# Kernel optimization log

Hardware: AMD Instinct MI355X
Metric: run time of the kernel (lower is better)

The kernel has to match this reference:

```python
import jax, jax.numpy as jnp
import numpy as np

D_IN = 1024
D_OUT = 1024
NUM_HEADS = 16
HEAD_DIM = D_OUT // NUM_HEADS


def setup_inputs() -> dict:
    key = jax.random.key(0)
    ks = jax.random.split(key, 6)
    scale = 0.02
    x = jax.random.normal(ks[0], (2, 2048, D_IN), dtype=jnp.float32)
    Wq = jax.random.normal(ks[1], (D_IN, D_OUT), dtype=jnp.float32) * scale
    Wk = jax.random.normal(ks[2], (D_IN, D_OUT), dtype=jnp.float32) * scale
    Wv = jax.random.normal(ks[3], (D_IN, D_OUT), dtype=jnp.float32) * scale
    Wo = jax.random.normal(ks[4], (D_OUT, D_OUT), dtype=jnp.float32) * scale
    bo = jax.random.normal(ks[5], (D_OUT,), dtype=jnp.float32) * scale
    return {"x": x, "Wq": Wq, "Wk": Wk, "Wv": Wv, "Wo": Wo, "bo": bo}


def reference(x, Wq, Wk, Wv, Wo, bo):
    b, T, _ = x.shape
    h, dh = NUM_HEADS, HEAD_DIM
    # QKV projections (no bias), split heads: [b,T,d_out] -> [b,h,T,dh]
    q = (x @ Wq).reshape(b, T, h, dh).transpose(0, 2, 1, 3)
    k = (x @ Wk).reshape(b, T, h, dh).transpose(0, 2, 1, 3)
    v = (x @ Wv).reshape(b, T, h, dh).transpose(0, 2, 1, 3)
    # scaled dot-product scores with causal mask
    scores = jnp.einsum("bhqd,bhkd->bhqk", q, k) / jnp.sqrt(jnp.float32(dh))
    causal = jnp.tril(jnp.ones((T, T), dtype=bool))  # True = allowed
    scores = jnp.where(causal, scores, -jnp.inf)
    attn = jax.nn.softmax(scores, axis=-1)
    # dropout p=0.0 -> identity
    ctx = jnp.einsum("bhqk,bhkd->bhqd", attn, v)
    ctx = ctx.transpose(0, 2, 1, 3).reshape(b, T, h * dh)
    return ctx @ Wo + bo
```

## Files before the change

### kernel.cpp

```cpp
#include <hip/hip_runtime.h>

typedef __attribute__((ext_vector_type(8))) __bf16 bf16x8;
typedef __attribute__((ext_vector_type(4))) __bf16 bf16x4;
typedef __attribute__((ext_vector_type(4))) float  f32x4;

static constexpr int TSEQ    = 2048;
static constexpr int DMODEL  = 1024;
static constexpr int HD      = 64;
static constexpr int VSTRIDE = 2080;
static constexpr int LSTR    = 72;

#define AS1 __attribute__((address_space(1)))
#define AS3 __attribute__((address_space(3)))

__global__ __launch_bounds__(256) void k_prep(const float* __restrict__ x,
    const float* __restrict__ w0, const float* __restrict__ w1,
    const float* __restrict__ w2, const float* __restrict__ w3,
    __bf16* __restrict__ xbf, __bf16* __restrict__ wt_all) {
  __shared__ float tile[32][33];
  const int blk = blockIdx.x;
  const int tid = threadIdx.x;
  if (blk < 4096) {
    size_t i = ((size_t)blk * 256 + tid) * 4;
    float4 v = *(const float4*)(x + i);
    bf16x4 o = { (__bf16)v.x, (__bf16)v.y, (__bf16)v.z, (__bf16)v.w };
    *(bf16x4*)(xbf + i) = o;
    return;
  }
  const int tz = blk - 4096;
  const int wi = tz >> 10;
  const int tl = tz & 1023;
  const int n0 = (tl & 31) * 32, k0 = (tl >> 5) * 32;
  const float* w = wi == 0 ? w0 : wi == 1 ? w1 : wi == 2 ? w2 : w3;
  __bf16* out = wt_all + (size_t)wi * DMODEL * DMODEL;
  const int tx = tid & 31, ty0 = (tid >> 5) * 4;
#pragma unroll
  for (int j = 0; j < 4; j++)
    tile[ty0 + j][tx] = w[(size_t)(k0 + ty0 + j) * DMODEL + n0 + tx];
  __syncthreads();
#pragma unroll
  for (int j = 0; j < 4; j++)
    out[(size_t)(n0 + ty0 + j) * DMODEL + k0 + tx] = (__bf16)tile[tx][ty0 + j];
}

template <int NB>
__device__ __forceinline__ void gemm_mainloop_p(const __bf16* __restrict__ A,
                                                const __bf16* __restrict__ Bt,
                                                int bm, int bn,
                                                __bf16* At, __bf16* Bl,
                                                f32x4 acc[4][NB / 32]) {
  constexpr int NT = NB / 32;
  const int tid  = threadIdx.x;
  const int lane = tid & 63;
  const int l15  = lane & 15, quad = lane >> 4;
  const int wv   = tid >> 6;
  const int wm   = (wv >> 1) * 64, wn = (wv & 1) * (NT * 16);
  const int srow = lane >> 2;
  const int scol = (((lane & 3) ^ ((lane >> 3) & 3)) << 3);
  const int rsw  = (l15 >> 1) & 3;

  auto stage = [&](int k0, int hb) {
#pragma unroll
    for (int ss = 0; ss < 2; ss++) {
      const int s   = wv * 2 + ss;
      const int row = s * 16 + srow;
      __builtin_amdgcn_global_load_lds(
          (const AS1 void*)(A + (size_t)(bm + row) * 1024 + k0 + scol),
          (AS3 void*)(At + hb * 4096 + s * 512), 16, 0, 0);
    }
#pragma unroll
    for (int ss = 0; ss < NB / 64; ss++) {
      const int s   = wv * (NB / 64) + ss;
      const int row = s * 16 + srow;
      __builtin_amdgcn_global_load_lds(
          (const AS1 void*)(Bt + (size_t)(bn + row) * 1024 + k0 + scol),
          (AS3 void*)(Bl + hb * (NB * 32) + s * 512), 16, 0, 0);
    }
  };

  stage(0, 0);
  for (int k0 = 0; k0 < 1024; k0 += 32) {
    const int cur = (k0 >> 5) & 1;
    __syncthreads();
    bf16x8 af[4], bfr[NT];
#pragma unroll
    for (int mt = 0; mt < 4; mt++)
      af[mt] = *(const bf16x8*)(At + cur * 4096 + (wm + mt * 16 + l15) * 32 +
                                ((quad ^ rsw) << 3));
#pragma unroll
    for (int nt = 0; nt < NT; nt++)
      bfr[nt] = *(const bf16x8*)(Bl + cur * (NB * 32) + (wn + nt * 16 + l15) * 32 +
                                 ((quad ^ rsw) << 3));
    if (k0 + 32 < 1024) stage(k0 + 32, cur ^ 1);
#pragma unroll
    for (int mt = 0; mt < 4; mt++)
#pragma unroll
      for (int nt = 0; nt < NT; nt++)
        acc[mt][nt] = __builtin_amdgcn_mfma_f32_16x16x32_bf16(
            af[mt], bfr[nt], acc[mt][nt], 0, 0, 0);
  }
}

__global__ __launch_bounds__(256) void k_gemm_qkv(const __bf16* __restrict__ xbf,
    const __bf16* __restrict__ wt_all, __bf16* __restrict__ qws,
    __bf16* __restrict__ kws, __bf16* __restrict__ vtws) {
  __shared__ __bf16 At[2 * 128 * 32];
  __shared__ __bf16 Bl[2 * 128 * 32];
  const int which = blockIdx.z;
  const __bf16* wt = wt_all + (size_t)which * DMODEL * DMODEL;
  const int bm = blockIdx.y * 128, bn = blockIdx.x * 128;
  f32x4 acc[4][4];
  const f32x4 z = {0.f, 0.f, 0.f, 0.f};
#pragma unroll
  for (int mt = 0; mt < 4; mt++)
#pragma unroll
    for (int nt = 0; nt < 4; nt++) acc[mt][nt] = z;
  gemm_mainloop_p<128>(xbf, wt, bm, bn, At, Bl, acc);
  const int lane = threadIdx.x & 63;
  const int l15 = lane & 15, quad = lane >> 4;
  const int wv = threadIdx.x >> 6;
  const int wm = (wv >> 1) * 64, wn = (wv & 1) * 64;
  if (which == 2) {
#pragma unroll
    for (int mt = 0; mt < 4; mt++)
#pragma unroll
      for (int nt = 0; nt < 4; nt++) {
        int t0 = bm + wm + mt * 16 + quad * 4;
        int n = bn + wn + nt * 16 + l15;
        int h = n >> 6, d = n & 63;
        int b = t0 >> 11;
        int bh = b * 16 + h;
        bf16x4 o = { (__bf16)acc[mt][nt][0], (__bf16)acc[mt][nt][1],
                     (__bf16)acc[mt][nt][2], (__bf16)acc[mt][nt][3] };
        *(bf16x4*)(vtws + ((size_t)bh * HD + d) * VSTRIDE + (t0 & 2047)) = o;
      }
  } else {
#pragma unroll
    for (int mt = 0; mt < 4; mt++)
#pragma unroll
      for (int nt = 0; nt < 4; nt++)
#pragma unroll
        for (int r = 0; r < 4; r++) {
          int m = bm + wm + mt * 16 + quad * 4 + r;
          int n = bn + wn + nt * 16 + l15;
          int b = m >> 11, t = m & 2047;
          int h = n >> 6,  d = n & 63;
          int bh = b * 16 + h;
          float av = acc[mt][nt][r];
          if (which == 0) qws[((size_t)bh * TSEQ + t) * HD + d] = (__bf16)(av * 0.18033688f);
          else            kws[((size_t)bh * TSEQ + t) * HD + d] = (__bf16)av;
        }
  }
}

__global__ __launch_bounds__(256) void k_attn(const __bf16* __restrict__ qws,
    const __bf16* __restrict__ kws, const __bf16* __restrict__ vtws,
    __bf16* __restrict__ ctx) {
  const int bh  = blockIdx.x & 31;
  const int qb0 = blockIdx.x >> 5, qb1 = 31 - qb0;
  const int tid = threadIdx.x;
  const int lane = tid & 63, wv = tid >> 6;
  const int l15 = lane & 15, quad = lane >> 4;
  const __bf16* qp = qws  + (size_t)bh * TSEQ * HD;
  const __bf16* kp = kws  + (size_t)bh * TSEQ * HD;
  const __bf16* vp = vtws + (size_t)bh * HD * VSTRIDE;
  const int b = bh >> 4, h = bh & 15;

  __shared__ __bf16 kbuf[2][64 * LSTR];
  __shared__ __bf16 vbuf[2][64 * LSTR];
  __shared__ __bf16 plds[4][16 * LSTR];

  const f32x4 z = {0.f, 0.f, 0.f, 0.f};
  const int sr = tid >> 3, sc = (tid & 7) * 8;

  const int qr0a = qb0 * 64 + wv * 16;
  const int qr0b = qb1 * 64 + wv * 16;
  bf16x8 aq0[2], aq1[2];
#pragma unroll
  for (int kb = 0; kb < 2; kb++) {
    aq0[kb] = *(const bf16x8*)(qp + (size_t)(qr0a + l15) * HD + kb * 32 + quad * 8);
    aq1[kb] = *(const bf16x8*)(qp + (size_t)(qr0b + l15) * HD + kb * 32 + quad * 8);
  }

  bf16x8 kreg[2], vreg[2];
  kreg[0] = *(const bf16x8*)(kp + (size_t)sr * HD + sc);
  kreg[1] = *(const bf16x8*)(kp + (size_t)(sr + 32) * HD + sc);
  vreg[0] = *(const bf16x8*)(vp + (size_t)sr * VSTRIDE + sc);
  vreg[1] = *(const bf16x8*)(vp + (size_t)(sr + 32) * VSTRIDE + sc);
  *(bf16x8*)(kbuf[0] + sr * LSTR + sc)        = kreg[0];
  *(bf16x8*)(kbuf[0] + (sr + 32) * LSTR + sc) = kreg[1];
  *(bf16x8*)(vbuf[0] + sr * LSTR + sc)        = vreg[0];
  *(bf16x8*)(vbuf[0] + (sr + 32) * LSTR + sc) = vreg[1];
  __syncthreads();

  float lpart[4] = {0.f, 0.f, 0.f, 0.f};
  f32x4 acc[4];
#pragma unroll
  for (int dt = 0; dt < 4; dt++) acc[dt] = z;

  for (int s = 0; s < 33; s++) {
    const int cur = s & 1;
    const bool h0 = (s <= qb0);
    const bool masked = (s == qb0) || (s == 32);

    if (s + 1 < 33) {
      const int ktn = (s + 1 <= qb0) ? (s + 1) * 64 : (s - qb0) * 64;
      kreg[0] = *(const bf16x8*)(kp + (size_t)(ktn + sr) * HD + sc);
      kreg[1] = *(const bf16x8*)(kp + (size_t)(ktn + sr + 32) * HD + sc);
      vreg[0] = *(const bf16x8*)(vp + (size_t)sr * VSTRIDE + ktn + sc);
      vreg[1] = *(const bf16x8*)(vp + (size_t)(sr + 32) * VSTRIDE + ktn + sc);
    }

    const __bf16* kb_ = kbuf[cur];
    const __bf16* vb_ = vbuf[cur];
    f32x4 sarr[4];
#pragma unroll
    for (int nt = 0; nt < 4; nt++) sarr[nt] = z;
#pragma unroll
    for (int nt = 0; nt < 4; nt++)
#pragma unroll
      for (int kb = 0; kb < 2; kb++) {
        bf16x8 bk = *(const bf16x8*)(kb_ + (nt * 16 + l15) * LSTR + kb * 32 + quad * 8);
        bf16x8 a  = h0 ? aq0[kb] : aq1[kb];
        sarr[nt] = __builtin_amdgcn_mfma_f32_16x16x32_bf16(a, bk, sarr[nt], 0, 0, 0);
      }
    if (masked) {
#pragma unroll
      for (int r = 0; r < 4; r++) {
        const int qloc = wv * 16 + quad * 4 + r;
#pragma unroll
        for (int nt = 0; nt < 4; nt++) {
          int kloc = nt * 16 + l15;
          float p = (kloc <= qloc) ? __builtin_amdgcn_exp2f(sarr[nt][r]) : 0.f;
          lpart[r] += p;
          plds[wv][(quad * 4 + r) * LSTR + nt * 16 + l15] = (__bf16)p;
        }
      }
    } else {
#pragma unroll
      for (int r = 0; r < 4; r++)
#pragma unroll
        for (int nt = 0; nt < 4; nt++) {
          float p = __builtin_amdgcn_exp2f(sarr[nt][r]);
          lpart[r] += p;
          plds[wv][(quad * 4 + r) * LSTR + nt * 16 + l15] = (__bf16)p;
        }
    }
#pragma unroll
    for (int kb = 0; kb < 2; kb++) {
      bf16x8 ap = *(const bf16x8*)(&plds[wv][l15 * LSTR + kb * 32 + quad * 8]);
#pragma unroll
      for (int dt = 0; dt < 4; dt++) {
        bf16x8 bvv = *(const bf16x8*)(vb_ + (dt * 16 + l15) * LSTR + kb * 32 + quad * 8);
        acc[dt] = __builtin_amdgcn_mfma_f32_16x16x32_bf16(ap, bvv, acc[dt], 0, 0, 0);
      }
    }

    if (s + 1 < 33) {
      const int nxt = cur ^ 1;
      *(bf16x8*)(kbuf[nxt] + sr * LSTR + sc)        = kreg[0];
      *(bf16x8*)(kbuf[nxt] + (sr + 32) * LSTR + sc) = kreg[1];
      *(bf16x8*)(vbuf[nxt] + sr * LSTR + sc)        = vreg[0];
      *(bf16x8*)(vbuf[nxt] + (sr + 32) * LSTR + sc) = vreg[1];
    }
    __syncthreads();

    if (masked) {
      const int qr0 = h0 ? qr0a : qr0b;
#pragma unroll
      for (int r = 0; r < 4; r++) {
        float l = lpart[r];
        l += __shfl_xor(l, 1, 64);
        l += __shfl_xor(l, 2, 64);
        l += __shfl_xor(l, 4, 64);
        l += __shfl_xor(l, 8, 64);
        float linv = 1.f / l;
        const int qrow = qr0 + quad * 4 + r;
#pragma unroll
        for (int dt = 0; dt < 4; dt++)
          ctx[((size_t)(b * TSEQ + qrow)) * DMODEL + h * 64 + dt * 16 + l15] =
              (__bf16)(acc[dt][r] * linv);
        lpart[r] = 0.f;
      }
#pragma unroll
      for (int dt = 0; dt < 4; dt++) acc[dt] = z;
    }
  }
}

__global__ __launch_bounds__(256) void k_gemm_out(const __bf16* __restrict__ ctx,
    const __bf16* __restrict__ wot, const float* __restrict__ bo,
    float* __restrict__ out) {
  __shared__ __bf16 At[2 * 128 * 32];
  __shared__ __bf16 Bl[2 * 64 * 32];
  const int bm = blockIdx.y * 128, bn = blockIdx.x * 64;
  f32x4 acc[4][2];
  const f32x4 z = {0.f, 0.f, 0.f, 0.f};
#pragma unroll
  for (int mt = 0; mt < 4; mt++)
#pragma unroll
    for (int nt = 0; nt < 2; nt++) acc[mt][nt] = z;
  gemm_mainloop_p<64>(ctx, wot, bm, bn, At, Bl, acc);
  const int lane = threadIdx.x & 63;
  const int l15 = lane & 15, quad = lane >> 4;
  const int wv = threadIdx.x >> 6;
  const int wm = (wv >> 1) * 64, wn = (wv & 1) * 32;
#pragma unroll
  for (int mt = 0; mt < 4; mt++)
#pragma unroll
    for (int nt = 0; nt < 2; nt++)
#pragma unroll
      for (int r = 0; r < 4; r++) {
        int m = bm + wm + mt * 16 + quad * 4 + r;
        int n = bn + wn + nt * 16 + l15;
        out[(size_t)m * DMODEL + n] = acc[mt][nt][r] + bo[n];
      }
}

extern "C" void kernel_launch(void* const* d_in, const int* in_sizes, int n_in,
                              void* d_out, int out_size, void* d_ws, size_t ws_size,
                              hipStream_t stream) {
  const float* x  = (const float*)d_in[0];
  const float* Wq = (const float*)d_in[1];
  const float* Wk = (const float*)d_in[2];
  const float* Wv = (const float*)d_in[3];
  const float* Wo = (const float*)d_in[4];
  const float* bo = (const float*)d_in[5];
  float* out = (float*)d_out;

  __bf16* xbf  = (__bf16*)d_ws;
  __bf16* wt   = xbf  + (size_t)4096 * 1024;
  __bf16* qws  = wt   + (size_t)4 * 1024 * 1024;
  __bf16* kws  = qws  + (size_t)32 * 2048 * 64;
  __bf16* vtws = kws  + (size_t)32 * 2048 * 64;
  __bf16* ctx  = xbf;

  k_prep<<<8192, 256, 0, stream>>>(x, Wq, Wk, Wv, Wo, xbf, wt);
  k_gemm_qkv<<<dim3(8, 32, 3), 256, 0, stream>>>(xbf, wt, qws, kws, vtws);
  k_attn<<<512, 256, 0, stream>>>(qws, kws, vtws, ctx);
  k_gemm_out<<<dim3(16, 32), 256, 0, stream>>>(ctx, wt + (size_t)3 * 1024 * 1024, bo, out);
}
```

Baseline: 177.6 us.

## Triple-buffer GEMM LDS staging with vmcnt waits and swizzle attention P tile

Result: no change. 180.4 us (+1.6%).

```diff
diff --git a/kernel.cpp b/kernel.cpp
--- a/kernel.cpp
+++ b/kernel.cpp
@@ -44,7 +44,7 @@
 }
 
 template <int NB>
-__device__ __forceinline__ void gemm_mainloop_p(const __bf16* __restrict__ A,
+__device__ __forceinline__ void gemm_mainloop_r(const __bf16* __restrict__ A,
                                                 const __bf16* __restrict__ Bt,
                                                 int bm, int bn,
                                                 __bf16* At, __bf16* Bl,
@@ -59,14 +59,14 @@
   const int scol = (((lane & 3) ^ ((lane >> 3) & 3)) << 3);
   const int rsw  = (l15 >> 1) & 3;
 
-  auto stage = [&](int k0, int hb) {
+  auto stage = [&](int k0, int rb) {
 #pragma unroll
     for (int ss = 0; ss < 2; ss++) {
       const int s   = wv * 2 + ss;
       const int row = s * 16 + srow;
       __builtin_amdgcn_global_load_lds(
           (const AS1 void*)(A + (size_t)(bm + row) * 1024 + k0 + scol),
-          (AS3 void*)(At + hb * 4096 + s * 512), 16, 0, 0);
+          (AS3 void*)(At + rb * 4096 + s * 512), 16, 0, 0);
     }
 #pragma unroll
     for (int ss = 0; ss < NB / 64; ss++) {
@@ -74,38 +74,48 @@
       const int row = s * 16 + srow;
       __builtin_amdgcn_global_load_lds(
           (const AS1 void*)(Bt + (size_t)(bn + row) * 1024 + k0 + scol),
-          (AS3 void*)(Bl + hb * (NB * 32) + s * 512), 16, 0, 0);
+          (AS3 void*)(Bl + rb * (NB * 32) + s * 512), 16, 0, 0);
     }
   };
 
   stage(0, 0);
+  int rb = 0;
   for (int k0 = 0; k0 < 1024; k0 += 32) {
-    const int cur = (k0 >> 5) & 1;
-    __syncthreads();
+    const int nrb = (rb == 2) ? 0 : rb + 1;
+    if (k0 + 32 < 1024) {
+      stage(k0 + 32, nrb);
+      if constexpr (NB == 128) asm volatile("s_waitcnt vmcnt(4)" ::: "memory");
+      else                     asm volatile("s_waitcnt vmcnt(3)" ::: "memory");
+    } else {
+      asm volatile("s_waitcnt vmcnt(0)" ::: "memory");
+    }
+    asm volatile("s_waitcnt lgkmcnt(0)" ::: "memory");
+    __builtin_amdgcn_sched_barrier(0);
+    __builtin_amdgcn_s_barrier();
     bf16x8 af[4], bfr[NT];
 #pragma unroll
     for (int mt = 0; mt < 4; mt++)
-      af[mt] = *(const bf16x8*)(At + cur * 4096 + (wm + mt * 16 + l15) * 32 +
+      af[mt] = *(const bf16x8*)(At + rb * 4096 + (wm + mt * 16 + l15) * 32 +
                                 ((quad ^ rsw) << 3));
 #pragma unroll
     for (int nt = 0; nt < NT; nt++)
-      bfr[nt] = *(const bf16x8*)(Bl + cur * (NB * 32) + (wn + nt * 16 + l15) * 32 +
+      bfr[nt] = *(const bf16x8*)(Bl + rb * (NB * 32) + (wn + nt * 16 + l15) * 32 +
                                  ((quad ^ rsw) << 3));
-    if (k0 + 32 < 1024) stage(k0 + 32, cur ^ 1);
 #pragma unroll
     for (int mt = 0; mt < 4; mt++)
 #pragma unroll
       for (int nt = 0; nt < NT; nt++)
         acc[mt][nt] = __builtin_amdgcn_mfma_f32_16x16x32_bf16(
             af[mt], bfr[nt], acc[mt][nt], 0, 0, 0);
+    rb = nrb;
   }
 }
 
 __global__ __launch_bounds__(256) void k_gemm_qkv(const __bf16* __restrict__ xbf,
     const __bf16* __restrict__ wt_all, __bf16* __restrict__ qws,
     __bf16* __restrict__ kws, __bf16* __restrict__ vtws) {
-  __shared__ __bf16 At[2 * 128 * 32];
-  __shared__ __bf16 Bl[2 * 128 * 32];
+  __shared__ __bf16 At[3 * 128 * 32];
+  __shared__ __bf16 Bl[3 * 128 * 32];
   const int which = blockIdx.z;
   const __bf16* wt = wt_all + (size_t)which * DMODEL * DMODEL;
   const int bm = blockIdx.y * 128, bn = blockIdx.x * 128;
@@ -115,7 +125,7 @@
   for (int mt = 0; mt < 4; mt++)
 #pragma unroll
     for (int nt = 0; nt < 4; nt++) acc[mt][nt] = z;
-  gemm_mainloop_p<128>(xbf, wt, bm, bn, At, Bl, acc);
+  gemm_mainloop_r<128>(xbf, wt, bm, bn, At, Bl, acc);
   const int lane = threadIdx.x & 63;
   const int l15 = lane & 15, quad = lane >> 4;
   const int wv = threadIdx.x >> 6;
@@ -233,7 +243,7 @@
           int kloc = nt * 16 + l15;
           float p = (kloc <= qloc) ? __builtin_amdgcn_exp2f(sarr[nt][r]) : 0.f;
           lpart[r] += p;
-          plds[wv][(quad * 4 + r) * LSTR + nt * 16 + l15] = (__bf16)p;
+          plds[wv][(quad * 4 + r) * LSTR + ((nt ^ quad) * 16) + l15] = (__bf16)p;
         }
       }
     } else {
@@ -243,12 +253,13 @@
         for (int nt = 0; nt < 4; nt++) {
           float p = __builtin_amdgcn_exp2f(sarr[nt][r]);
           lpart[r] += p;
-          plds[wv][(quad * 4 + r) * LSTR + nt * 16 + l15] = (__bf16)p;
+          plds[wv][(quad * 4 + r) * LSTR + ((nt ^ quad) * 16) + l15] = (__bf16)p;
         }
     }
 #pragma unroll
     for (int kb = 0; kb < 2; kb++) {
-      bf16x8 ap = *(const bf16x8*)(&plds[wv][l15 * LSTR + kb * 32 + quad * 8]);
+      const int pch = (2 * kb + (quad >> 1)) ^ (l15 >> 2);
+      bf16x8 ap = *(const bf16x8*)(&plds[wv][l15 * LSTR + pch * 16 + (quad & 1) * 8]);
 #pragma unroll
       for (int dt = 0; dt < 4; dt++) {
         bf16x8 bvv = *(const bf16x8*)(vb_ + (dt * 16 + l15) * LSTR + kb * 32 + quad * 8);
@@ -291,8 +302,8 @@
 __global__ __launch_bounds__(256) void k_gemm_out(const __bf16* __restrict__ ctx,
     const __bf16* __restrict__ wot, const float* __restrict__ bo,
     float* __restrict__ out) {
-  __shared__ __bf16 At[2 * 128 * 32];
-  __shared__ __bf16 Bl[2 * 64 * 32];
+  __shared__ __bf16 At[3 * 128 * 32];
+  __shared__ __bf16 Bl[3 * 64 * 32];
   const int bm = blockIdx.y * 128, bn = blockIdx.x * 64;
   f32x4 acc[4][2];
   const f32x4 z = {0.f, 0.f, 0.f, 0.f};
@@ -300,7 +311,7 @@
   for (int mt = 0; mt < 4; mt++)
 #pragma unroll
     for (int nt = 0; nt < 2; nt++) acc[mt][nt] = z;
-  gemm_mainloop_p<64>(ctx, wot, bm, bn, At, Bl, acc);
+  gemm_mainloop_r<64>(ctx, wot, bm, bn, At, Bl, acc);
   const int lane = threadIdx.x & 63;
   const int l15 = lane & 15, quad = lane >> 4;
   const int wv = threadIdx.x >> 6;
```
